# Kernel tuning notes

Hardware: AMD Instinct MI355X
Metric: run time of the kernel (lower is better)

## Reference

```python
import jax, jax.numpy as jnp
import numpy as np

B, N, D, DP = 8, 4096, 512, 512  # batch, tokens, d, d_prime (hidden of MLP == d)


def setup_inputs() -> dict:
    key = jax.random.key(0)
    ks = jax.random.split(key, 9)
    def w(k, out_f, in_f):
        # torch Linear default init ~ U(-1/sqrt(in), 1/sqrt(in)); use scaled normal
        return jax.random.normal(k, (out_f, in_f), jnp.float32) / np.sqrt(in_f).astype(np.float32)
    return {
        "X": jax.random.normal(ks[0], (B, N, D), jnp.float32),
        # MLP1: Linear(d, d) -> GELU -> Linear(d, d_prime)
        "W1a": w(ks[1], D, D),  "b1a": jnp.zeros((D,), jnp.float32),
        "W1b": w(ks[2], DP, D), "b1b": jnp.zeros((DP,), jnp.float32),
        # MLP2 (tied=False): same structure
        "W2a": w(ks[3], D, D),  "b2a": jnp.zeros((D,), jnp.float32),
        "W2b": w(ks[4], DP, D), "b2b": jnp.zeros((DP,), jnp.float32),
    }


def _mlp(x, Wa, ba, Wb, bb):
    # Linear -> GELU(exact, erf-based like torch default) -> Linear
    h = jax.nn.gelu(x @ Wa.T + ba, approximate=False)
    return h @ Wb.T + bb


def reference(X, W1a, b1a, W1b, b1b, W2a, b2a, W2b, b2b):
    W1 = _mlp(X, W1a, b1a, W1b, b1b)        # [b, n, d_prime]
    W2 = _mlp(X, W2a, b2a, W2b, b2b)        # [b, n, d_prime]
    P = jnp.einsum('bnp,bnd->bpd', W1, X)   # [b, d_prime, d]
    A = jax.nn.gelu(P, approximate=False)
    Y = jnp.einsum('bnp,bpd->bnd', W2, A)   # [b, n, d]
    return Y
```

## Files before the change

kernel.cpp:

```cpp
#include <hip/hip_runtime.h>
#include <hip/hip_bf16.h>

typedef __attribute__((ext_vector_type(8))) short short8;
typedef __attribute__((ext_vector_type(4))) short short4v;
typedef __attribute__((ext_vector_type(4))) float floatx4;

__device__ __forceinline__ void gload_lds16(const void* g, void* l) {
  __builtin_amdgcn_global_load_lds(
      (const __attribute__((address_space(1))) void*)g,
      (__attribute__((address_space(3))) void*)l, 16, 0, 0);
}

__device__ __forceinline__ float gelu_fast(float x) {
  float z = 1.5957691216f * (x + 0.044715f * x * x * x);
  float e = __expf(-z);
  return x * __builtin_amdgcn_rcpf(1.0f + e);
}

#define FENCE() asm volatile("" ::: "memory")

template<bool HASBIAS, bool OUT_F32>
__device__ __forceinline__
void gemm128_core(const __hip_bfloat16* __restrict__ A,
                  const __hip_bfloat16* __restrict__ B,
                  const float* __restrict__ bias,
                  void* __restrict__ C,
                  int bx, int by)
{
  __shared__ __align__(16) __hip_bfloat16 SB[2][2 * 128 * 64];

  const int tid  = threadIdx.x;
  const int lane = tid & 63;
  const int wid  = tid >> 6;
  const int wr   = wid >> 2;
  const int wc   = wid & 3;
  const int brow = by * 128;
  const int bcol = bx * 128;

  floatx4 acc[4][2];
#pragma unroll
  for (int i = 0; i < 4; i++)
#pragma unroll
    for (int j = 0; j < 2; j++) acc[i][j] = (floatx4){0.f, 0.f, 0.f, 0.f};

  const int srow  = tid >> 3;
  const int skoff = (((tid & 7) ^ (srow & 7))) * 8;

  auto STAGE = [&](int buf, int kt) {
    const int k0 = kt * 64;
#pragma unroll
    for (int r = 0; r < 2; ++r) {
      gload_lds16(A + (size_t)(brow + r * 64 + srow) * 512 + k0 + skoff,
                  (void*)(&SB[buf][0] + r * 4096 + tid * 8));
      gload_lds16(B + (size_t)(bcol + r * 64 + srow) * 512 + k0 + skoff,
                  (void*)(&SB[buf][8192] + r * 4096 + tid * 8));
    }
  };

  const int rs0 = (((lane >> 4)) ^ (lane & 7)) * 8;
  const int rs1 = ((4 + (lane >> 4)) ^ (lane & 7)) * 8;

  STAGE(0, 0);
  asm volatile("s_waitcnt vmcnt(0)" ::: "memory");
  __builtin_amdgcn_s_barrier();
  FENCE();

  for (int kt = 0; kt < 8; ++kt) {
    const int cur = kt & 1;
    if (kt < 7) STAGE(cur ^ 1, kt + 1);
    const __hip_bfloat16* As = &SB[cur][0];
    const __hip_bfloat16* Bs = &SB[cur][8192];
    __builtin_amdgcn_s_setprio(1);
#pragma unroll
    for (int kk = 0; kk < 2; ++kk) {
      const int rs = kk ? rs1 : rs0;
      short8 a[4], b[2];
#pragma unroll
      for (int i = 0; i < 4; i++)
        a[i] = *(const short8*)(As + (wr * 64 + i * 16 + (lane & 15)) * 64 + rs);
#pragma unroll
      for (int j = 0; j < 2; j++)
        b[j] = *(const short8*)(Bs + (wc * 32 + j * 16 + (lane & 15)) * 64 + rs);
#pragma unroll
      for (int i = 0; i < 4; i++)
#pragma unroll
        for (int j = 0; j < 2; j++)
          acc[i][j] = __builtin_amdgcn_mfma_f32_16x16x32_bf16(a[i], b[j], acc[i][j], 0, 0, 0);
    }
    __builtin_amdgcn_s_setprio(0);

    if (kt < 7) {
      asm volatile("s_waitcnt vmcnt(0)" ::: "memory");
      __builtin_amdgcn_s_barrier();
      FENCE();
    }
  }

#pragma unroll
  for (int i = 0; i < 4; i++) {
    const int row0 = brow + wr * 64 + i * 16 + (lane >> 4) * 4;
#pragma unroll
    for (int j = 0; j < 2; j++) {
      const int col = bcol + wc * 32 + j * 16 + (lane & 15);
      const float bv = HASBIAS ? bias[col] : 0.f;
#pragma unroll
      for (int r = 0; r < 4; r++) {
        float v = acc[i][j][r] + bv;
        if (OUT_F32)
          ((float*)C)[(size_t)(row0 + r) * 512 + col] = v;
        else
          ((__hip_bfloat16*)C)[(size_t)(row0 + r) * 512 + col] = __float2bfloat16(v);
      }
    }
  }
}

__device__ __forceinline__ void swz_chunked(int gx, int gy, int total,
                                            int& bx, int& by, int& bz) {
  const int f = blockIdx.x + gx * (blockIdx.y + gy * blockIdx.z);
  const int l = (f & 7) * (total >> 3) + (f >> 3);
  bx = l % gx;
  const int rr = l / gx;
  by = rr % gy;
  bz = rr / gy;
}

__global__ __launch_bounds__(512, 2)
void g128_h12(const __hip_bfloat16* Xb,
              const __hip_bfloat16* W1a, const __hip_bfloat16* W2a,
              const float* b1a, const float* b2a,
              __hip_bfloat16* H1, __hip_bfloat16* H2) {
  int bx, by, bz;
  swz_chunked(4, 256, 2048, bx, by, bz);
  const __hip_bfloat16* B = bz ? W2a : W1a;
  const float* bias       = bz ? b2a : b1a;
  __hip_bfloat16* C       = bz ? H2 : H1;
  gemm128_core<true, false>(Xb, B, bias, C, bx, by);
}
__global__ __launch_bounds__(512, 2)
void g128_w12(const __hip_bfloat16* H1, const __hip_bfloat16* H2,
              const __hip_bfloat16* W1b, const __hip_bfloat16* W2b,
              const float* b1b, const float* b2b,
              __hip_bfloat16* W1n, __hip_bfloat16* W2m) {
  int bx, by, bz;
  swz_chunked(4, 256, 2048, bx, by, bz);
  const __hip_bfloat16* A = bz ? H2 : H1;
  const __hip_bfloat16* B = bz ? W2b : W1b;
  const float* bias       = bz ? b2b : b1b;
  __hip_bfloat16* C       = bz ? W2m : W1n;
  gemm128_core<true, false>(A, B, bias, C, bx, by);
}
__global__ __launch_bounds__(512, 2)
void g128_w1(const __hip_bfloat16* A, const __hip_bfloat16* B, const float* bias,
             __hip_bfloat16* C) {
  int bx, by, bz;
  swz_chunked(4, 256, 1024, bx, by, bz);
  gemm128_core<true, false>(A, B, bias, C, bx, by);
}
__global__ __launch_bounds__(512, 2)
void g128_w2(const __hip_bfloat16* A, const __hip_bfloat16* B, const float* bias,
             __hip_bfloat16* C) {
  int bx, by, bz;
  swz_chunked(4, 256, 1024, bx, by, bz);
  gemm128_core<true, false>(A, B, bias, C, bx, by);
}
__global__ __launch_bounds__(512, 2)
void g128_y(const __hip_bfloat16* A, const __hip_bfloat16* B, float* C) {
  int bx, by, bz;
  swz_chunked(4, 32, 1024, bx, by, bz);
  gemm128_core<false, true>(A + (size_t)bz * 4096 * 512,
                            B + (size_t)bz * 262144, nullptr,
                            C + (size_t)bz * 4096 * 512, bx, by);
}

__global__ __launch_bounds__(512, 2)
void g128_p(const __hip_bfloat16* __restrict__ Ag,
            const __hip_bfloat16* __restrict__ Bg,
            __hip_bfloat16* __restrict__ Cg)
{
  const int f = blockIdx.x + 4 * (blockIdx.y + 4 * blockIdx.z);
  const int xcd = f & 7, s = f >> 3;
  const int zq = xcd + 8 * (s >> 4);
  const int t  = s & 15;
  const int by = t >> 2;
  const int bx = t & 3;

  const __hip_bfloat16* A = Ag + (size_t)zq * 2 * 262144;
  const __hip_bfloat16* B = Bg + (size_t)zq * 2 * 262144;
  __hip_bfloat16*       C = Cg + (size_t)zq * 262144;

  __shared__ __align__(16) __hip_bfloat16 SB[2][2 * 128 * 64];

  const int tid  = threadIdx.x;
  const int lane = tid & 63;
  const int wid  = tid >> 6;
  const int wr   = wid >> 2;
  const int wc   = wid & 3;
  const int brow = by * 128;
  const int bcol = bx * 128;

  floatx4 acc[4][2];
#pragma unroll
  for (int i = 0; i < 4; i++)
#pragma unroll
    for (int j = 0; j < 2; j++) acc[i][j] = (floatx4){0.f, 0.f, 0.f, 0.f};

  const int srow  = tid >> 3;
  const int skoff = (((tid & 7) ^ (srow & 7))) * 8;

  auto STAGE = [&](int buf, int kt) {
    const size_t cb = (size_t)(kt >> 3) * 262144;
    const int k0 = (kt & 7) * 64;
#pragma unroll
    for (int r = 0; r < 2; ++r) {
      gload_lds16(A + cb + (size_t)(brow + r * 64 + srow) * 512 + k0 + skoff,
                  (void*)(&SB[buf][0] + r * 4096 + tid * 8));
      gload_lds16(B + cb + (size_t)(bcol + r * 64 + srow) * 512 + k0 + skoff,
                  (void*)(&SB[buf][8192] + r * 4096 + tid * 8));
    }
  };

  const int rs0 = (((lane >> 4)) ^ (lane & 7)) * 8;
  const int rs1 = ((4 + (lane >> 4)) ^ (lane & 7)) * 8;

  STAGE(0, 0);
  asm volatile("s_waitcnt vmcnt(0)" ::: "memory");
  __builtin_amdgcn_s_barrier();
  FENCE();

  for (int kt = 0; kt < 16; ++kt) {
    const int cur = kt & 1;
    if (kt < 15) STAGE(cur ^ 1, kt + 1);
    const __hip_bfloat16* As = &SB[cur][0];
    const __hip_bfloat16* Bs = &SB[cur][8192];
    __builtin_amdgcn_s_setprio(1);
#pragma unroll
    for (int kk = 0; kk < 2; ++kk) {
      const int rs = kk ? rs1 : rs0;
      short8 a[4], b[2];
#pragma unroll
      for (int i = 0; i < 4; i++)
        a[i] = *(const short8*)(As + (wr * 64 + i * 16 + (lane & 15)) * 64 + rs);
#pragma unroll
      for (int j = 0; j < 2; j++)
        b[j] = *(const short8*)(Bs + (wc * 32 + j * 16 + (lane & 15)) * 64 + rs);
#pragma unroll
      for (int i = 0; i < 4; i++)
#pragma unroll
        for (int j = 0; j < 2; j++)
          acc[i][j] = __builtin_amdgcn_mfma_f32_16x16x32_bf16(a[i], b[j], acc[i][j], 0, 0, 0);
    }
    __builtin_amdgcn_s_setprio(0);

    if (kt < 15) {
      asm volatile("s_waitcnt vmcnt(0)" ::: "memory");
      __builtin_amdgcn_s_barrier();
      FENCE();
    }
  }

#pragma unroll
  for (int i = 0; i < 4; i++) {
    const int row0 = brow + wr * 64 + i * 16 + (lane >> 4) * 4;
#pragma unroll
    for (int j = 0; j < 2; j++) {
      const int col = bcol + wc * 32 + j * 16 + (lane & 15);
#pragma unroll
      for (int r = 0; r < 4; r++)
        C[(size_t)(row0 + r) * 512 + col] = __float2bfloat16(acc[i][j][r]);
    }
  }
}

__global__ __launch_bounds__(256)
void gelu_inplace(__hip_bfloat16* __restrict__ H, long n) {
  long i = ((long)blockIdx.x * 256 + threadIdx.x) * 8;
  if (i >= n) return;
  short8 v = *(const short8*)(H + i);
  short8 o;
#pragma unroll
  for (int j = 0; j < 8; j++) {
    float x = __bfloat162float(((const __hip_bfloat16*)&v)[j]);
    ((__hip_bfloat16*)&o)[j] = __float2bfloat16(gelu_fast(x));
  }
  *(short8*)(H + i) = o;
}

__global__ __launch_bounds__(256)
void cvt_w4(const float* __restrict__ w0, const float* __restrict__ w1,
            const float* __restrict__ w2, const float* __restrict__ w3,
            __hip_bfloat16* __restrict__ o0, __hip_bfloat16* __restrict__ o1,
            __hip_bfloat16* __restrict__ o2, __hip_bfloat16* __restrict__ o3) {
  const int sel = blockIdx.x >> 7;
  const float* in = sel == 0 ? w0 : sel == 1 ? w1 : sel == 2 ? w2 : w3;
  __hip_bfloat16* out = sel == 0 ? o0 : sel == 1 ? o1 : sel == 2 ? o2 : o3;
  const long i = (((long)(blockIdx.x & 127)) * 256 + threadIdx.x) * 8;
  float4 v0 = *(const float4*)(in + i);
  float4 v1 = *(const float4*)(in + i + 4);
  short8 o;
  __hip_bfloat16* ob = (__hip_bfloat16*)&o;
  ob[0] = __float2bfloat16(v0.x); ob[1] = __float2bfloat16(v0.y);
  ob[2] = __float2bfloat16(v0.z); ob[3] = __float2bfloat16(v0.w);
  ob[4] = __float2bfloat16(v1.x); ob[5] = __float2bfloat16(v1.y);
  ob[6] = __float2bfloat16(v1.z); ob[7] = __float2bfloat16(v1.w);
  *(short8*)(out + i) = o;
}

__global__ __launch_bounds__(256)
void cvt_x_xt(const float* __restrict__ X,
              __hip_bfloat16* __restrict__ Xb,
              __hip_bfloat16* __restrict__ XT)
{
  __shared__ __hip_bfloat16 t[64][66];
  const int b  = blockIdx.z;
  const int n0 = blockIdx.y * 64;
  const int d0 = blockIdx.x * 64;
  const float* I = X + (size_t)b * 4096 * 512;
  __hip_bfloat16* XB = Xb + (size_t)b * 4096 * 512;
  __hip_bfloat16* XO = XT + ((size_t)b * 8 + (n0 >> 9)) * 512 * 512;
  const int nl0 = n0 & 511;
  const int tid = threadIdx.x;
#pragma unroll
  for (int it = 0; it < 4; ++it) {
    const int idx = it * 256 + tid;
    const int r   = idx >> 4;
    const int c4  = (idx & 15) * 4;
    float4 v = *(const float4*)&I[(size_t)(n0 + r) * 512 + d0 + c4];
    short4v o;
    __hip_bfloat16* ob = (__hip_bfloat16*)&o;
    ob[0] = __float2bfloat16(v.x); ob[1] = __float2bfloat16(v.y);
    ob[2] = __float2bfloat16(v.z); ob[3] = __float2bfloat16(v.w);
    t[r][c4]     = ob[0]; t[r][c4 + 1] = ob[1];
    t[r][c4 + 2] = ob[2]; t[r][c4 + 3] = ob[3];
    *(short4v*)&XB[(size_t)(n0 + r) * 512 + d0 + c4] = o;
  }
  __syncthreads();
#pragma unroll
  for (int it = 0; it < 4; ++it) {
    const int idx = it * 256 + tid;
    const int dr  = idx >> 4;
    const int n4  = (idx & 15) * 4;
    short4v o;
    __hip_bfloat16* ob = (__hip_bfloat16*)&o;
#pragma unroll
    for (int j = 0; j < 4; j++) ob[j] = t[n4 + j][dr];
    *(short4v*)&XO[(size_t)(d0 + dr) * 512 + nl0 + n4] = o;
  }
}

__global__ __launch_bounds__(256)
void transpose_w1(const __hip_bfloat16* __restrict__ in,
                  __hip_bfloat16* __restrict__ out)
{
  __shared__ __hip_bfloat16 t[64][66];
  const int b  = blockIdx.z;
  const int n0 = blockIdx.y * 64;
  const int p0 = blockIdx.x * 64;
  const __hip_bfloat16* I = in + (size_t)b * 4096 * 512;
  __hip_bfloat16* O = out + ((size_t)b * 8 + (n0 >> 9)) * 512 * 512;
  const int nl0 = n0 & 511;
  const int tid = threadIdx.x;
#pragma unroll
  for (int it = 0; it < 2; ++it) {
    const int idx = it * 256 + tid;
    const int r   = idx >> 3;
    const int c8  = (idx & 7) * 8;
    short8 v = *(const short8*)&I[(size_t)(n0 + r) * 512 + p0 + c8];
#pragma unroll
    for (int j = 0; j < 8; j++) t[r][c8 + j] = ((const __hip_bfloat16*)&v)[j];
  }
  __syncthreads();
#pragma unroll
  for (int it = 0; it < 2; ++it) {
    const int idx = it * 256 + tid;
    const int dr  = idx >> 3;
    const int n8  = (idx & 7) * 8;
    short8 o;
#pragma unroll
    for (int j = 0; j < 8; j++) ((__hip_bfloat16*)&o)[j] = t[n8 + j][dr];
    *(short8*)&O[(size_t)(p0 + dr) * 512 + nl0 + n8] = o;
  }
}

__global__ __launch_bounds__(256)
void reduce_gelu_bf16(const __hip_bfloat16* __restrict__ part,
                      __hip_bfloat16* __restrict__ AT) {
  const long o = ((long)blockIdx.x * 256 + threadIdx.x) * 8;
  const long b = o >> 18;
  const long i = o & 262143;
  float s[8] = {0.f, 0.f, 0.f, 0.f, 0.f, 0.f, 0.f, 0.f};
#pragma unroll
  for (int q = 0; q < 4; q++) {
    short8 v = *(const short8*)(part + (((b << 2) + q) << 18) + i);
#pragma unroll
    for (int j = 0; j < 8; j++) s[j] += __bfloat162float(((const __hip_bfloat16*)&v)[j]);
  }
  short8 o8;
#pragma unroll
  for (int j = 0; j < 8; j++)
    ((__hip_bfloat16*)&o8)[j] = __float2bfloat16(gelu_fast(s[j]));
  *(short8*)(AT + o) = o8;
}

extern "C" void kernel_launch(void* const* d_in, const int* in_sizes, int n_in,
                              void* d_out, int out_size, void* d_ws, size_t ws_size,
                              hipStream_t stream) {
  const float* X   = (const float*)d_in[0];
  const float* W1a = (const float*)d_in[1];
  const float* b1a = (const float*)d_in[2];
  const float* W1b = (const float*)d_in[3];
  const float* b1b = (const float*)d_in[4];
  const float* W2a = (const float*)d_in[5];
  const float* b2a = (const float*)d_in[6];
  const float* W2b = (const float*)d_in[7];
  const float* b2b = (const float*)d_in[8];
  float* Y = (float*)d_out;

  char* ws = (char*)d_ws;
  const size_t SZ = 33554432;
  __hip_bfloat16* R0 = (__hip_bfloat16*)(ws);
  __hip_bfloat16* R1 = (__hip_bfloat16*)(ws + SZ);
  __hip_bfloat16* R2 = (__hip_bfloat16*)(ws + 2 * SZ);
  __hip_bfloat16* R3 = (__hip_bfloat16*)(ws + 3 * SZ);
  __hip_bfloat16* AT = (__hip_bfloat16*)(ws + 4 * SZ);
  __hip_bfloat16* Wb = (__hip_bfloat16*)(ws + 4 * SZ + 4194304);
  __hip_bfloat16* R4 = (__hip_bfloat16*)(ws + 4 * SZ + 6291456);
  const bool big_ws = ws_size >= (4 * SZ + 6291456 + SZ);
  __hip_bfloat16* W1ab = Wb;
  __hip_bfloat16* W1bb = Wb + 262144;
  __hip_bfloat16* W2ab = Wb + 2 * 262144;
  __hip_bfloat16* W2bb = Wb + 3 * 262144;

  dim3 blk(256), blk512(512);

  cvt_w4<<<512, blk, 0, stream>>>(W1a, W1b, W2a, W2b, W1ab, W1bb, W2ab, W2bb);
  __hip_bfloat16* Xb  = R0;
  __hip_bfloat16* XTc = R3;
  cvt_x_xt<<<dim3(8, 64, 8), blk, 0, stream>>>(X, Xb, XTc);

  __hip_bfloat16* H1 = R1;
  __hip_bfloat16* H2 = R2;
  g128_h12<<<dim3(4, 256, 2), blk512, 0, stream>>>(Xb, W1ab, W2ab, b1a, b2a, H1, H2);
  gelu_inplace<<<16384, blk, 0, stream>>>(H1, 33554432L);

  if (big_ws) {
    __hip_bfloat16* W1n = R0;
    __hip_bfloat16* W2m = R4;
    g128_w12<<<dim3(4, 256, 2), blk512, 0, stream>>>(H1, H2, W1bb, W2bb, b1b, b2b, W1n, W2m);
    __hip_bfloat16* W1Tc = R1;
    transpose_w1<<<dim3(8, 64, 8), blk, 0, stream>>>(W1n, W1Tc);
    __hip_bfloat16* part = R2;
    g128_p<<<dim3(4, 4, 32), blk512, 0, stream>>>(XTc, W1Tc, part);
    reduce_gelu_bf16<<<1024, blk, 0, stream>>>(part, AT);
    g128_y<<<dim3(4, 32, 8), blk512, 0, stream>>>(W2m, AT, Y);
  } else {
    __hip_bfloat16* W1n = R0;
    g128_w1<<<dim3(4, 256, 1), blk512, 0, stream>>>(H1, W1bb, b1b, W1n);
    __hip_bfloat16* W1Tc = R1;
    transpose_w1<<<dim3(8, 64, 8), blk, 0, stream>>>(W1n, W1Tc);
    __hip_bfloat16* part = R0;
    g128_p<<<dim3(4, 4, 32), blk512, 0, stream>>>(XTc, W1Tc, part);
    reduce_gelu_bf16<<<1024, blk, 0, stream>>>(part, AT);
    __hip_bfloat16* W2m = R3;
    g128_w2<<<dim3(4, 256, 1), blk512, 0, stream>>>(H2, W2bb, b2b, W2m);
    g128_y<<<dim3(4, 32, 8), blk512, 0, stream>>>(W2m, AT, Y);
  }
}
```

Measured before the change: 186.5 us.

## Make each MLP GEMM block sweep all four column tiles for its row panel

Adds a GEMM core in which each 128-row block loops over the four 128-column output tiles and prefetches the next tile's first K-slice across tile boundaries. The H12 and W12 launches shrink from 2048 to 512 blocks. The intent is to cut per-block launch and prologue cost and to keep the A row panel hot in cache. The trade-off is fewer blocks for the machine's compute units, which may leave CUs underfilled and gives worse load balance.

```diff
diff --git a/kernel.cpp b/kernel.cpp
--- a/kernel.cpp
+++ b/kernel.cpp
@@ -18,6 +18,112 @@
 }
 
 #define FENCE() asm volatile("" ::: "memory")
+
+template<bool HASBIAS, bool OUT_F32>
+__device__ __forceinline__
+void gemm128_p4_core(const __hip_bfloat16* __restrict__ A,
+                     const __hip_bfloat16* __restrict__ B,
+                     const float* __restrict__ bias,
+                     void* __restrict__ C,
+                     int by)
+{
+  __shared__ __align__(16) __hip_bfloat16 SB[2][2 * 128 * 64];
+
+  const int tid  = threadIdx.x;
+  const int lane = tid & 63;
+  const int wid  = tid >> 6;
+  const int wr   = wid >> 2;
+  const int wc   = wid & 3;
+  const int brow = by * 128;
+
+  const int srow  = tid >> 3;
+  const int skoff = (((tid & 7) ^ (srow & 7))) * 8;
+
+  auto STAGE = [&](int buf, int kt, int bcol) {
+    const int k0 = kt * 64;
+#pragma unroll
+    for (int r = 0; r < 2; ++r) {
+      gload_lds16(A + (size_t)(brow + r * 64 + srow) * 512 + k0 + skoff,
+                  (void*)(&SB[buf][0] + r * 4096 + tid * 8));
+      gload_lds16(B + (size_t)(bcol + r * 64 + srow) * 512 + k0 + skoff,
+                  (void*)(&SB[buf][8192] + r * 4096 + tid * 8));
+    }
+  };
+
+  const int rs0 = (((lane >> 4)) ^ (lane & 7)) * 8;
+  const int rs1 = ((4 + (lane >> 4)) ^ (lane & 7)) * 8;
+
+  STAGE(0, 0, 0);
+  asm volatile("s_waitcnt vmcnt(0)" ::: "memory");
+  __builtin_amdgcn_s_barrier();
+  FENCE();
+
+#pragma unroll 1
+  for (int t = 0; t < 4; ++t) {
+    const int bcol = t * 128;
+    floatx4 acc[4][2];
+#pragma unroll
+    for (int i = 0; i < 4; i++)
+#pragma unroll
+      for (int j = 0; j < 2; j++) acc[i][j] = (floatx4){0.f, 0.f, 0.f, 0.f};
+
+    for (int kt = 0; kt < 8; ++kt) {
+      const int cur = kt & 1;
+      if (kt < 7)      STAGE(cur ^ 1, kt + 1, bcol);
+      else if (t < 3)  STAGE(cur ^ 1, 0, bcol + 128);
+      const __hip_bfloat16* As = &SB[cur][0];
+      const __hip_bfloat16* Bs = &SB[cur][8192];
+      __builtin_amdgcn_s_setprio(1);
+#pragma unroll
+      for (int kk = 0; kk < 2; ++kk) {
+        const int rs = kk ? rs1 : rs0;
+        short8 a[4], b[2];
+#pragma unroll
+        for (int i = 0; i < 4; i++)
+          a[i] = *(const short8*)(As + (wr * 64 + i * 16 + (lane & 15)) * 64 + rs);
+#pragma unroll
+        for (int j = 0; j < 2; j++)
+          b[j] = *(const short8*)(Bs + (wc * 32 + j * 16 + (lane & 15)) * 64 + rs);
+#pragma unroll
+        for (int i = 0; i < 4; i++)
+#pragma unroll
+          for (int j = 0; j < 2; j++)
+            acc[i][j] = __builtin_amdgcn_mfma_f32_16x16x32_bf16(a[i], b[j], acc[i][j], 0, 0, 0);
+      }
+      __builtin_amdgcn_s_setprio(0);
+
+      if (kt < 7) {
+        asm volatile("s_waitcnt vmcnt(0)" ::: "memory");
+        __builtin_amdgcn_s_barrier();
+        FENCE();
+      }
+    }
+
+#pragma unroll
+    for (int i = 0; i < 4; i++) {
+      const int row0 = brow + wr * 64 + i * 16 + (lane >> 4) * 4;
+#pragma unroll
+      for (int j = 0; j < 2; j++) {
+        const int col = bcol + wc * 32 + j * 16 + (lane & 15);
+        const float bv = HASBIAS ? bias[col] : 0.f;
+#pragma unroll
+        for (int r = 0; r < 4; r++) {
+          float v = acc[i][j][r] + bv;
+          if (OUT_F32)
+            ((float*)C)[(size_t)(row0 + r) * 512 + col] = v;
+          else
+            ((__hip_bfloat16*)C)[(size_t)(row0 + r) * 512 + col] = __float2bfloat16(v);
+        }
+      }
+    }
+
+    if (t < 3) {
+      asm volatile("s_waitcnt vmcnt(0)" ::: "memory");
+      __builtin_amdgcn_s_barrier();
+      FENCE();
+    }
+  }
+}
 
 template<bool HASBIAS, bool OUT_F32>
 __device__ __forceinline__
@@ -130,25 +236,29 @@
               const __hip_bfloat16* W1a, const __hip_bfloat16* W2a,
               const float* b1a, const float* b2a,
               __hip_bfloat16* H1, __hip_bfloat16* H2) {
-  int bx, by, bz;
-  swz_chunked(4, 256, 2048, bx, by, bz);
+  const int f = blockIdx.y + 256 * blockIdx.z;
+  const int l = (f & 7) * 64 + (f >> 3);
+  const int by = l & 255;
+  const int bz = l >> 8;
   const __hip_bfloat16* B = bz ? W2a : W1a;
   const float* bias       = bz ? b2a : b1a;
   __hip_bfloat16* C       = bz ? H2 : H1;
-  gemm128_core<true, false>(Xb, B, bias, C, bx, by);
+  gemm128_p4_core<true, false>(Xb, B, bias, C, by);
 }
 __global__ __launch_bounds__(512, 2)
 void g128_w12(const __hip_bfloat16* H1, const __hip_bfloat16* H2,
               const __hip_bfloat16* W1b, const __hip_bfloat16* W2b,
               const float* b1b, const float* b2b,
               __hip_bfloat16* W1n, __hip_bfloat16* W2m) {
-  int bx, by, bz;
-  swz_chunked(4, 256, 2048, bx, by, bz);
+  const int f = blockIdx.y + 256 * blockIdx.z;
+  const int l = (f & 7) * 64 + (f >> 3);
+  const int by = l & 255;
+  const int bz = l >> 8;
   const __hip_bfloat16* A = bz ? H2 : H1;
   const __hip_bfloat16* B = bz ? W2b : W1b;
   const float* bias       = bz ? b2b : b1b;
   __hip_bfloat16* C       = bz ? W2m : W1n;
-  gemm128_core<true, false>(A, B, bias, C, bx, by);
+  gemm128_p4_core<true, false>(A, B, bias, C, by);
 }
 __global__ __launch_bounds__(512, 2)
 void g128_w1(const __hip_bfloat16* A, const __hip_bfloat16* B, const float* bias,
@@ -440,13 +550,13 @@
 
   __hip_bfloat16* H1 = R1;
   __hip_bfloat16* H2 = R2;
-  g128_h12<<<dim3(4, 256, 2), blk512, 0, stream>>>(Xb, W1ab, W2ab, b1a, b2a, H1, H2);
+  g128_h12<<<dim3(1, 256, 2), blk512, 0, stream>>>(Xb, W1ab, W2ab, b1a, b2a, H1, H2);
   gelu_inplace<<<16384, blk, 0, stream>>>(H1, 33554432L);
 
   if (big_ws) {
     __hip_bfloat16* W1n = R0;
     __hip_bfloat16* W2m = R4;
-    g128_w12<<<dim3(4, 256, 2), blk512, 0, stream>>>(H1, H2, W1bb, W2bb, b1b, b2b, W1n, W2m);
+    g128_w12<<<dim3(1, 256, 2), blk512, 0, stream>>>(H1, H2, W1bb, W2bb, b1b, b2b, W1n, W2m);
     __hip_bfloat16* W1Tc = R1;
     transpose_w1<<<dim3(8, 64, 8), blk, 0, stream>>>(W1n, W1Tc);
     __hip_bfloat16* part = R2;
```

Result: slower. 212.4 us (+13.9%).
